# Optimization experiments

Hardware: AMD Instinct MI355X
Metric: run time of the kernel (lower is better)

## Reference

```python
import jax, jax.numpy as jnp
import numpy as np

B, M, E, H, TOPK = 1024, 10000, 8, 512, 2


def setup_inputs() -> dict:
    key = jax.random.key(0)
    ks = jax.random.split(key, 6)
    s_in = 1.0 / np.sqrt(M)
    s_h = 1.0 / np.sqrt(H)
    x = jax.random.normal(ks[0], (B, M), dtype=jnp.float32)
    # Expert params, torch Linear layout stacked over experts
    W1 = jax.random.uniform(ks[1], (E, H, M), jnp.float32, -s_in, s_in)
    b1 = jax.random.uniform(ks[2], (E, H), jnp.float32, -s_in, s_in)
    W2 = jax.random.uniform(ks[3], (E, M, H), jnp.float32, -s_h, s_h)
    b2 = jax.random.uniform(ks[4], (E, M), jnp.float32, -s_h, s_h)
    Wr = jax.random.uniform(ks[5], (E, M), jnp.float32, -s_in, s_in)  # router, no bias
    return {"x": x, "W1": W1, "b1": b1, "W2": W2, "b2": b2, "Wr": Wr}


def reference(x, W1, b1, W2, b2, Wr):
    # Router: logits [B, E], sparse top-k softmax weights scattered to dense [B, E]
    logits = jnp.einsum('bm,em->be', x, Wr)
    topk_vals, topk_idx = jax.lax.top_k(logits, TOPK)
    probs = jax.nn.softmax(topk_vals, axis=-1)
    rw = jnp.zeros_like(logits).at[jnp.arange(B)[:, None], topk_idx].set(probs)
    # Dense all-expert MLP (faithful to original: every expert runs on every token)
    h = jax.nn.relu(jnp.einsum('bm,ehm->beh', x, W1) + b1)      # [B, E, H]
    eo = jnp.einsum('beh,emh->bem', h, W2) + b2                  # [B, E, M]
    # Masked weighted combine
    out = jnp.sum(rw[:, :, None] * eo, axis=1)                   # [B, M]
    return out
```

## Files before the change

kernel.cpp:

```cpp
#include <hip/hip_runtime.h>
#include <hip/hip_bf16.h>


#define B_TOK 1024
#define M_DIM 10000
#define E_NUM 8
#define H_DIM 512
#define NSTEP 313

typedef __attribute__((ext_vector_type(4))) float fx4;
typedef __attribute__((ext_vector_type(8))) short sx8;
typedef __attribute__((ext_vector_type(4))) short sx4;

#define LSTR 40
#define BUFS (256 * LSTR)

__device__ __forceinline__ short f2bf(float f) {
  union { __hip_bfloat16 h; short s; } u;
  u.h = __float2bfloat16(f);
  return u.s;
}

__device__ __forceinline__ sx8 pack8(fx4 a, fx4 b) {
  sx8 r;
  r[0] = f2bf(a[0]); r[1] = f2bf(a[1]); r[2] = f2bf(a[2]); r[3] = f2bf(a[3]);
  r[4] = f2bf(b[0]); r[5] = f2bf(b[1]); r[6] = f2bf(b[2]); r[7] = f2bf(b[3]);
  return r;
}

__global__ void k_zero(int* cnt, int* cnt2) {
  if (threadIdx.x < E_NUM) cnt[threadIdx.x] = 0;
  if (threadIdx.x < 2 * E_NUM) cnt2[threadIdx.x] = 0;
}

__global__ __launch_bounds__(256) void k_router(
    const float* __restrict__ x, const float* __restrict__ Wr,
    int* __restrict__ cnt, int* __restrict__ cnt2,
    int* __restrict__ tokAll, int* __restrict__ qlist2, float* __restrict__ wlist2)
{
  int b = blockIdx.x, t = threadIdx.x;
  const float* xr = x + (size_t)b * M_DIM;
  double acc[E_NUM];
#pragma unroll
  for (int e = 0; e < E_NUM; e++) acc[e] = 0.0;
  for (int m = t; m < M_DIM; m += 256) {
    float xv = xr[m];
#pragma unroll
    for (int e = 0; e < E_NUM; e++)
      acc[e] += (double)xv * (double)Wr[e * M_DIM + m];
  }
#pragma unroll
  for (int e = 0; e < E_NUM; e++) {
#pragma unroll
    for (int off = 32; off > 0; off >>= 1)
      acc[e] += __shfl_xor(acc[e], off);
  }
  __shared__ double part[4][E_NUM];
  int wave = t >> 6;
  if ((t & 63) == 0) {
    for (int e = 0; e < E_NUM; e++) part[wave][e] = acc[e];
  }
  __syncthreads();
  if (t == 0) {
    double lg[E_NUM];
    for (int e = 0; e < E_NUM; e++)
      lg[e] = part[0][e] + part[1][e] + part[2][e] + part[3][e];
    int i0 = 0;
    for (int e = 1; e < E_NUM; e++) if (lg[e] > lg[i0]) i0 = e;
    int i1 = (i0 == 0) ? 1 : 0;
    for (int e = 0; e < E_NUM; e++) if (e != i0 && lg[e] > lg[i1]) i1 = e;
    double ex = exp(lg[i1] - lg[i0]);
    float p0 = (float)(1.0 / (1.0 + ex));
    float p1 = (float)(ex / (1.0 + ex));
    int q0 = atomicAdd(&cnt[i0], 1);
    tokAll[i0 * B_TOK + q0] = b;
    int j0 = atomicAdd(&cnt2[i0 * 2 + 0], 1);
    qlist2[(i0 * 2 + 0) * B_TOK + j0] = q0;
    wlist2[(i0 * 2 + 0) * B_TOK + j0] = p0;
    int q1 = atomicAdd(&cnt[i1], 1);
    tokAll[i1 * B_TOK + q1] = b;
    int j1 = atomicAdd(&cnt2[i1 * 2 + 1], 1);
    qlist2[(i1 * 2 + 1) * B_TOK + j1] = q1;
    wlist2[(i1 * 2 + 1) * B_TOK + j1] = p1;
  }
}

__global__ __launch_bounds__(256) void k_mlp1(
    const float* __restrict__ x, const float* __restrict__ W1,
    const int* __restrict__ cnt, const int* __restrict__ tokAll,
    float* __restrict__ partials, int CH)
{
  int e = blockIdx.z;
  int tt = blockIdx.y >> 2, nt = blockIdx.y & 3;
  int kc = blockIdx.x;

  __shared__ int sh_ne, sh_eoff;
  __shared__ __align__(16) short SB[2 * BUFS];
  __shared__ int toks[128];

  int t = threadIdx.x;
  if (t == 0) {
    int off = 0;
    for (int k = 0; k < e; k++) off += cnt[k];
    sh_eoff = off; sh_ne = cnt[e];
  }
  __syncthreads();
  int ne = sh_ne, eoff = sh_eoff, row0 = tt * 128;
  if (row0 >= ne) return;
  int nvalid = min(128, ne - row0);

  if (t < 128) toks[t] = tokAll[e * B_TOK + row0 + min(t, nvalid - 1)];
  __syncthreads();

  int r4 = t >> 2, kch = t & 3;
  const float* xr0 = x + (size_t)toks[r4] * M_DIM;
  const float* xr1 = x + (size_t)toks[r4 + 64] * M_DIM;
  const float* wr0 = W1 + ((size_t)e * H_DIM + nt * 128 + r4) * M_DIM;
  const float* wr1 = W1 + ((size_t)e * H_DIM + nt * 128 + r4 + 64) * M_DIM;

  int lane = t & 63, wave = t >> 6;
  int wr = wave >> 1, wc = wave & 1;
  int lrow = lane & 15, khalf = lane >> 4;

  fx4 z4 = {0.f, 0.f, 0.f, 0.f};
  fx4 acc[4][4];
#pragma unroll
  for (int m = 0; m < 4; m++)
#pragma unroll
    for (int n = 0; n < 4; n++) acc[m][n] = z4;

  int s0 = kc * CH, s1 = min(s0 + CH, NSTEP);
  sx8 zv = {0, 0, 0, 0, 0, 0, 0, 0};

  {
    int off = s0 * 32 + kch * 8;
    int oc = min(off, M_DIM - 8);
    bool ok = (off + 8 <= M_DIM);
    fx4 A0 = *(const fx4*)(xr0 + oc), A0b = *(const fx4*)(xr0 + oc + 4);
    fx4 A1 = *(const fx4*)(xr1 + oc), A1b = *(const fx4*)(xr1 + oc + 4);
    fx4 B0 = *(const fx4*)(wr0 + oc), B0b = *(const fx4*)(wr0 + oc + 4);
    fx4 B1 = *(const fx4*)(wr1 + oc), B1b = *(const fx4*)(wr1 + oc + 4);
    sx8 pa0 = ok ? pack8(A0, A0b) : zv;
    sx8 pa1 = ok ? pack8(A1, A1b) : zv;
    sx8 pb0 = ok ? pack8(B0, B0b) : zv;
    sx8 pb1 = ok ? pack8(B1, B1b) : zv;
    *(sx8*)(&SB[r4 * LSTR + kch * 8]) = pa0;
    *(sx8*)(&SB[(r4 + 64) * LSTR + kch * 8]) = pa1;
    *(sx8*)(&SB[(128 + r4) * LSTR + kch * 8]) = pb0;
    *(sx8*)(&SB[(128 + r4 + 64) * LSTR + kch * 8]) = pb1;
  }
  __syncthreads();

  int c = 0;
  for (int s = s0; s < s1; s++) {
    int off = (s + 1) * 32 + kch * 8;
    int oc = min(off, M_DIM - 8);
    bool okn = (off + 8 <= M_DIM);
    fx4 A0 = *(const fx4*)(xr0 + oc), A0b = *(const fx4*)(xr0 + oc + 4);
    fx4 A1 = *(const fx4*)(xr1 + oc), A1b = *(const fx4*)(xr1 + oc + 4);
    fx4 B0 = *(const fx4*)(wr0 + oc), B0b = *(const fx4*)(wr0 + oc + 4);
    fx4 B1 = *(const fx4*)(wr1 + oc), B1b = *(const fx4*)(wr1 + oc + 4);

    int bo = c * BUFS;
    sx8 af[4], bf[4];
#pragma unroll
    for (int m = 0; m < 4; m++)
      af[m] = *(const sx8*)(&SB[bo + (wr * 64 + m * 16 + lrow) * LSTR + khalf * 8]);
#pragma unroll
    for (int n = 0; n < 4; n++)
      bf[n] = *(const sx8*)(&SB[bo + (128 + wc * 64 + n * 16 + lrow) * LSTR + khalf * 8]);
#pragma unroll
    for (int m = 0; m < 4; m++)
#pragma unroll
      for (int n = 0; n < 4; n++)
        acc[m][n] = __builtin_amdgcn_mfma_f32_16x16x32_bf16(af[m], bf[n], acc[m][n], 0, 0, 0);

    if (s + 1 < s1) {
      int wo = (c ^ 1) * BUFS;
      sx8 pa0 = okn ? pack8(A0, A0b) : zv;
      sx8 pa1 = okn ? pack8(A1, A1b) : zv;
      sx8 pb0 = okn ? pack8(B0, B0b) : zv;
      sx8 pb1 = okn ? pack8(B1, B1b) : zv;
      *(sx8*)(&SB[wo + r4 * LSTR + kch * 8]) = pa0;
      *(sx8*)(&SB[wo + (r4 + 64) * LSTR + kch * 8]) = pa1;
      *(sx8*)(&SB[wo + (128 + r4) * LSTR + kch * 8]) = pb0;
      *(sx8*)(&SB[wo + (128 + r4 + 64) * LSTR + kch * 8]) = pb1;
    }
    __syncthreads();
    c ^= 1;
  }

#pragma unroll
  for (int m = 0; m < 4; m++)
#pragma unroll
    for (int n = 0; n < 4; n++) {
      int colg = nt * 128 + wc * 64 + n * 16 + lrow;
#pragma unroll
      for (int r = 0; r < 4; r++) {
        int rl = wr * 64 + m * 16 + khalf * 4 + r;
        if (rl < nvalid) {
          int grow = eoff + row0 + rl;
          partials[((size_t)kc * 2048 + grow) * H_DIM + colg] = acc[m][n][r];
        }
      }
    }
}

__global__ __launch_bounds__(256) void k_hreduce(
    const float* __restrict__ partials, const float* __restrict__ b1,
    const int* __restrict__ cnt, short* __restrict__ hbuf, int KC)
{
  __shared__ int sc[E_NUM];
  int t = threadIdx.x;
  if (t < E_NUM) sc[t] = cnt[t];
  __syncthreads();
  int i = (blockIdx.x * 256 + t) * 4;
  int slot = i >> 9;
  int e = 0, off = 0;
  for (int k = 0; k < E_NUM - 1; k++) {
    if (slot >= off + sc[k]) { off += sc[k]; e++; } else break;
  }
  fx4 v = *(const fx4*)(partials + i);
  for (int kc = 1; kc < KC; kc++)
    v += *(const fx4*)(partials + (size_t)kc * 2048 * H_DIM + i);
  fx4 bv = *(const fx4*)(b1 + e * H_DIM + (i & (H_DIM - 1)));
  sx4 o;
#pragma unroll
  for (int j = 0; j < 4; j++) o[j] = f2bf(fmaxf(v[j] + bv[j], 0.f));
  *(sx4*)(hbuf + i) = o;
}

__global__ __launch_bounds__(256) void k_mlp2(
    const short* __restrict__ hbuf, const float* __restrict__ W2,
    const float* __restrict__ b2, const int* __restrict__ cnt,
    const int* __restrict__ cnt2, const int* __restrict__ tokAll,
    const int* __restrict__ qlist2, const float* __restrict__ wlist2,
    float* __restrict__ out, int ord)
{
  int e = blockIdx.z, mt = blockIdx.y, tt = blockIdx.x;

  __shared__ int sh_ne2, sh_eoff;
  __shared__ __align__(16) short SB[2 * BUFS];
  __shared__ int sl[128];
  __shared__ int tok2[128];
  __shared__ float wts[128];

  int t = threadIdx.x;
  if (t == 0) {
    int off = 0;
    for (int k = 0; k < e; k++) off += cnt[k];
    sh_eoff = off; sh_ne2 = cnt2[e * 2 + ord];
  }
  __syncthreads();
  int ne2 = sh_ne2, eoff = sh_eoff, row0 = tt * 128;
  if (row0 >= ne2) return;
  int nvalid = min(128, ne2 - row0);

  if (t < 128) {
    int j = row0 + min(t, nvalid - 1);
    int q = qlist2[(e * 2 + ord) * B_TOK + j];
    sl[t] = eoff + q;
    tok2[t] = tokAll[e * B_TOK + q];
    wts[t] = (t < nvalid) ? wlist2[(e * 2 + ord) * B_TOK + j] : 0.f;
  }
  __syncthreads();

  int r4 = t >> 2, kch = t & 3;
  const short* hr0 = hbuf + (size_t)sl[r4] * H_DIM;
  const short* hr1 = hbuf + (size_t)sl[r4 + 64] * H_DIM;
  const float* w20 = W2 + ((size_t)e * M_DIM + min(mt * 128 + r4, M_DIM - 1)) * H_DIM;
  const float* w21 = W2 + ((size_t)e * M_DIM + min(mt * 128 + r4 + 64, M_DIM - 1)) * H_DIM;

  int lane = t & 63, wave = t >> 6;
  int wr = wave >> 1, wc = wave & 1;
  int lrow = lane & 15, khalf = lane >> 4;

  fx4 z4 = {0.f, 0.f, 0.f, 0.f};
  fx4 acc[4][4];
#pragma unroll
  for (int m = 0; m < 4; m++)
#pragma unroll
    for (int n = 0; n < 4; n++) acc[m][n] = z4;

  {
    int off = kch * 8;
    sx8 pa0 = *(const sx8*)(hr0 + off);
    sx8 pa1 = *(const sx8*)(hr1 + off);
    fx4 B0 = *(const fx4*)(w20 + off), B0b = *(const fx4*)(w20 + off + 4);
    fx4 B1 = *(const fx4*)(w21 + off), B1b = *(const fx4*)(w21 + off + 4);
    *(sx8*)(&SB[r4 * LSTR + kch * 8]) = pa0;
    *(sx8*)(&SB[(r4 + 64) * LSTR + kch * 8]) = pa1;
    *(sx8*)(&SB[(128 + r4) * LSTR + kch * 8]) = pack8(B0, B0b);
    *(sx8*)(&SB[(128 + r4 + 64) * LSTR + kch * 8]) = pack8(B1, B1b);
  }
  __syncthreads();

  int c = 0;
  for (int s = 0; s < 16; s++) {
    int off = min((s + 1) * 32 + kch * 8, H_DIM - 8);
    sx8 pa0 = *(const sx8*)(hr0 + off);
    sx8 pa1 = *(const sx8*)(hr1 + off);
    fx4 B0 = *(const fx4*)(w20 + off), B0b = *(const fx4*)(w20 + off + 4);
    fx4 B1 = *(const fx4*)(w21 + off), B1b = *(const fx4*)(w21 + off + 4);

    int bo = c * BUFS;
    sx8 af[4], bf[4];
#pragma unroll
    for (int m = 0; m < 4; m++)
      af[m] = *(const sx8*)(&SB[bo + (wr * 64 + m * 16 + lrow) * LSTR + khalf * 8]);
#pragma unroll
    for (int n = 0; n < 4; n++)
      bf[n] = *(const sx8*)(&SB[bo + (128 + wc * 64 + n * 16 + lrow) * LSTR + khalf * 8]);
#pragma unroll
    for (int m = 0; m < 4; m++)
#pragma unroll
      for (int n = 0; n < 4; n++)
        acc[m][n] = __builtin_amdgcn_mfma_f32_16x16x32_bf16(af[m], bf[n], acc[m][n], 0, 0, 0);

    if (s + 1 < 16) {
      int wo = (c ^ 1) * BUFS;
      *(sx8*)(&SB[wo + r4 * LSTR + kch * 8]) = pa0;
      *(sx8*)(&SB[wo + (r4 + 64) * LSTR + kch * 8]) = pa1;
      *(sx8*)(&SB[wo + (128 + r4) * LSTR + kch * 8]) = pack8(B0, B0b);
      *(sx8*)(&SB[wo + (128 + r4 + 64) * LSTR + kch * 8]) = pack8(B1, B1b);
    }
    __syncthreads();
    c ^= 1;
  }

#pragma unroll
  for (int m = 0; m < 4; m++)
#pragma unroll
    for (int n = 0; n < 4; n++) {
      int colg = mt * 128 + wc * 64 + n * 16 + lrow;
      if (colg < M_DIM) {
        float b2v = b2[(size_t)e * M_DIM + colg];
#pragma unroll
        for (int r = 0; r < 4; r++) {
          int rl = wr * 64 + m * 16 + khalf * 4 + r;
          if (rl < nvalid) {
            float v = wts[rl] * (acc[m][n][r] + b2v);
            float* dst = out + (size_t)tok2[rl] * M_DIM + colg;
            if (ord == 0) *dst = v;
            else *dst += v;
          }
        }
      }
    }
}

extern "C" void kernel_launch(void* const* d_in, const int* in_sizes, int n_in,
                              void* d_out, int out_size, void* d_ws, size_t ws_size,
                              hipStream_t stream) {
  const float* x  = (const float*)d_in[0];
  const float* W1 = (const float*)d_in[1];
  const float* b1 = (const float*)d_in[2];
  const float* W2 = (const float*)d_in[3];
  const float* b2 = (const float*)d_in[4];
  const float* Wr = (const float*)d_in[5];
  float* out = (float*)d_out;

  int KC = (ws_size >= (size_t)36 * 1024 * 1024) ? 8 : 4;
  int CH = (NSTEP + KC - 1) / KC;

  char* p = (char*)d_ws;
  float* partials = (float*)p;               p += (size_t)KC * 2048 * H_DIM * 4;
  short* hbuf     = (short*)p;               p += (size_t)2048 * H_DIM * 2;
  int*   cnt      = (int*)p;                 p += 64;
  int*   cnt2     = (int*)p;                 p += 64;
  int*   tokAll   = (int*)p;                 p += E_NUM * B_TOK * 4;
  int*   qlist2   = (int*)p;                 p += 2 * E_NUM * B_TOK * 4;
  float* wlist2   = (float*)p;

  k_zero<<<1, 64, 0, stream>>>(cnt, cnt2);
  k_router<<<B_TOK, 256, 0, stream>>>(x, Wr, cnt, cnt2, tokAll, qlist2, wlist2);
  k_mlp1<<<dim3(KC, 12, E_NUM), 256, 0, stream>>>(x, W1, cnt, tokAll, partials, CH);
  k_hreduce<<<1024, 256, 0, stream>>>(partials, b1, cnt, hbuf, KC);
  k_mlp2<<<dim3(2, 79, E_NUM), 256, 0, stream>>>(hbuf, W2, b2, cnt, cnt2, tokAll,
                                                 qlist2, wlist2, out, 0);
  k_mlp2<<<dim3(2, 79, E_NUM), 256, 0, stream>>>(hbuf, W2, b2, cnt, cnt2, tokAll,
                                                 qlist2, wlist2, out, 1);
}
```

Baseline: 359.5 us.

## Pre-convert weights and activations to bf16 and load tiles via global_load_lds

When the workspace is large enough, x is converted to bf16 inside the router, and W1 and W2 are each converted to bf16 by a separate pass every call. New GEMM kernels then stream the bf16 tiles straight into LDS with global_load_lds double buffering, instead of converting fp32 to bf16 inside the MLP loops. This is meant to cut conversion work and register staging in the GEMM inner loops. In exchange it adds full fp32 read and bf16 write passes over roughly 330 MB of weights on every call, plus a large workspace requirement.

```diff
diff --git a/kernel.cpp b/kernel.cpp
--- a/kernel.cpp
+++ b/kernel.cpp
@@ -28,26 +28,54 @@
   return r;
 }
 
-__global__ void k_zero(int* cnt, int* cnt2) {
+__device__ __forceinline__ void gload16(const short* g, short* l) {
+  __builtin_amdgcn_global_load_lds(
+      (const __attribute__((address_space(1))) void*)g,
+      (__attribute__((address_space(3))) void*)l, 16, 0, 0);
+}
+
+__global__ void k_zero(int* cnt, int* cnt2, int* zpad) {
   if (threadIdx.x < E_NUM) cnt[threadIdx.x] = 0;
   if (threadIdx.x < 2 * E_NUM) cnt2[threadIdx.x] = 0;
+  if (threadIdx.x < 16) zpad[threadIdx.x] = 0;
+}
+
+__global__ __launch_bounds__(256) void k_cvt(
+    const float* __restrict__ src, short* __restrict__ dst)
+{
+  size_t i = ((size_t)blockIdx.x * 256 + threadIdx.x) * 8;
+  fx4 a = *(const fx4*)(src + i);
+  fx4 b = *(const fx4*)(src + i + 4);
+  *(sx8*)(dst + i) = pack8(a, b);
 }
 
 __global__ __launch_bounds__(256) void k_router(
     const float* __restrict__ x, const float* __restrict__ Wr,
     int* __restrict__ cnt, int* __restrict__ cnt2,
-    int* __restrict__ tokAll, int* __restrict__ qlist2, float* __restrict__ wlist2)
+    int* __restrict__ tokAll, int* __restrict__ qlist2, float* __restrict__ wlist2,
+    short* __restrict__ xb)
 {
   int b = blockIdx.x, t = threadIdx.x;
   const float* xr = x + (size_t)b * M_DIM;
   double acc[E_NUM];
 #pragma unroll
   for (int e = 0; e < E_NUM; e++) acc[e] = 0.0;
-  for (int m = t; m < M_DIM; m += 256) {
-    float xv = xr[m];
-#pragma unroll
-    for (int e = 0; e < E_NUM; e++)
-      acc[e] += (double)xv * (double)Wr[e * M_DIM + m];
+  if (xb) {
+    short* xbr = xb + (size_t)b * M_DIM;
+    for (int m = t; m < M_DIM; m += 256) {
+      float xv = xr[m];
+      xbr[m] = f2bf(xv);
+#pragma unroll
+      for (int e = 0; e < E_NUM; e++)
+        acc[e] += (double)xv * (double)Wr[e * M_DIM + m];
+    }
+  } else {
+    for (int m = t; m < M_DIM; m += 256) {
+      float xv = xr[m];
+#pragma unroll
+      for (int e = 0; e < E_NUM; e++)
+        acc[e] += (double)xv * (double)Wr[e * M_DIM + m];
+    }
   }
 #pragma unroll
   for (int e = 0; e < E_NUM; e++) {
@@ -85,6 +113,245 @@
   }
 }
 
+
+__global__ __launch_bounds__(256) void k_mlp1g(
+    const short* __restrict__ xb, const short* __restrict__ Wb,
+    const int* __restrict__ cnt, const int* __restrict__ tokAll,
+    float* __restrict__ partials, const short* __restrict__ zpad, int CH)
+{
+  int e = blockIdx.z;
+  int tt = blockIdx.y >> 2, nt = blockIdx.y & 3;
+  int kc = blockIdx.x;
+
+  __shared__ int sh_ne, sh_eoff;
+  __shared__ __align__(16) short LA[2][4096];
+  __shared__ __align__(16) short LB[2][4096];
+  __shared__ int toks[128];
+
+  int t = threadIdx.x;
+  if (t == 0) {
+    int off = 0;
+    for (int k = 0; k < e; k++) off += cnt[k];
+    sh_eoff = off; sh_ne = cnt[e];
+  }
+  __syncthreads();
+  int ne = sh_ne, eoff = sh_eoff, row0 = tt * 128;
+  if (row0 >= ne) return;
+  int nvalid = min(128, ne - row0);
+  if (t < 128) toks[t] = tokAll[e * B_TOK + row0 + min(t, nvalid - 1)];
+  __syncthreads();
+
+  int lane = t & 63, wave = t >> 6;
+  int srow = wave * 32 + (lane >> 2);
+  int scol = (lane & 3) * 8;
+  const short* ap0 = xb + (size_t)toks[srow] * M_DIM + scol;
+  const short* ap1 = xb + (size_t)toks[srow + 16] * M_DIM + scol;
+  const short* bp0 = Wb + ((size_t)e * H_DIM + nt * 128 + srow) * M_DIM + scol;
+  const short* bp1 = bp0 + (size_t)16 * M_DIM;
+  int ld0 = (wave * 32) * 32;
+  int ld1 = (wave * 32 + 16) * 32;
+
+  int wr = wave >> 1, wc = wave & 1;
+  int lrow = lane & 15, khalf = lane >> 4;
+
+  fx4 z4 = {0.f, 0.f, 0.f, 0.f};
+  fx4 acc[4][4];
+#pragma unroll
+  for (int m = 0; m < 4; m++)
+#pragma unroll
+    for (int n = 0; n < 4; n++) acc[m][n] = z4;
+
+  int s0 = kc * CH, s1 = min(s0 + CH, NSTEP);
+
+  {
+    int ko = s0 * 32;
+    bool ok = (ko + scol + 8 <= M_DIM);
+    gload16(ok ? (ap0 + ko) : zpad, LA[0] + ld0);
+    gload16(ok ? (ap1 + ko) : zpad, LA[0] + ld1);
+    gload16(ok ? (bp0 + ko) : zpad, LB[0] + ld0);
+    gload16(ok ? (bp1 + ko) : zpad, LB[0] + ld1);
+  }
+  __syncthreads();
+
+  int c = 0;
+  for (int s = s0; s < s1; s++) {
+    if (s + 1 < s1) {
+      int ko = (s + 1) * 32;
+      bool ok = (ko + scol + 8 <= M_DIM);
+      int cn = c ^ 1;
+      gload16(ok ? (ap0 + ko) : zpad, LA[cn] + ld0);
+      gload16(ok ? (ap1 + ko) : zpad, LA[cn] + ld1);
+      gload16(ok ? (bp0 + ko) : zpad, LB[cn] + ld0);
+      gload16(ok ? (bp1 + ko) : zpad, LB[cn] + ld1);
+    }
+    sx8 af[4], bf[4];
+#pragma unroll
+    for (int m = 0; m < 4; m++)
+      af[m] = *(const sx8*)(LA[c] + (wr * 64 + m * 16 + lrow) * 32 + khalf * 8);
+#pragma unroll
+    for (int n = 0; n < 4; n++)
+      bf[n] = *(const sx8*)(LB[c] + (wc * 64 + n * 16 + lrow) * 32 + khalf * 8);
+#pragma unroll
+    for (int m = 0; m < 4; m++)
+#pragma unroll
+      for (int n = 0; n < 4; n++)
+        acc[m][n] = __builtin_amdgcn_mfma_f32_16x16x32_bf16(af[m], bf[n], acc[m][n], 0, 0, 0);
+    __syncthreads();
+    c ^= 1;
+  }
+
+#pragma unroll
+  for (int m = 0; m < 4; m++)
+#pragma unroll
+    for (int n = 0; n < 4; n++) {
+      int colg = nt * 128 + wc * 64 + n * 16 + lrow;
+#pragma unroll
+      for (int r = 0; r < 4; r++) {
+        int rl = wr * 64 + m * 16 + khalf * 4 + r;
+        if (rl < nvalid) {
+          int grow = eoff + row0 + rl;
+          partials[((size_t)kc * 2048 + grow) * H_DIM + colg] = acc[m][n][r];
+        }
+      }
+    }
+}
+
+__global__ __launch_bounds__(256) void k_mlp2g(
+    const short* __restrict__ hbuf, const short* __restrict__ Wb,
+    const float* __restrict__ b2, const int* __restrict__ cnt,
+    const int* __restrict__ cnt2, const int* __restrict__ tokAll,
+    const int* __restrict__ qlist2, const float* __restrict__ wlist2,
+    float* __restrict__ out, int ord)
+{
+  int e = blockIdx.z, mt = blockIdx.y, tt = blockIdx.x;
+
+  __shared__ int sh_ne2, sh_eoff;
+  __shared__ __align__(16) short LA[2][4096];
+  __shared__ __align__(16) short LB[2][4096];
+  __shared__ int sl[128];
+  __shared__ int tok2[128];
+  __shared__ float wts[128];
+
+  int t = threadIdx.x;
+  if (t == 0) {
+    int off = 0;
+    for (int k = 0; k < e; k++) off += cnt[k];
+    sh_eoff = off; sh_ne2 = cnt2[e * 2 + ord];
+  }
+  __syncthreads();
+  int ne2 = sh_ne2, eoff = sh_eoff, row0 = tt * 128;
+  if (row0 >= ne2) return;
+  int nvalid = min(128, ne2 - row0);
+
+  if (t < 128) {
+    int j = row0 + min(t, nvalid - 1);
+    int q = qlist2[(e * 2 + ord) * B_TOK + j];
+    sl[t] = eoff + q;
+    tok2[t] = tokAll[e * B_TOK + q];
+    wts[t] = (t < nvalid) ? wlist2[(e * 2 + ord) * B_TOK + j] : 0.f;
+  }
+  __syncthreads();
+
+  int lane = t & 63, wave = t >> 6;
+  int srow = wave * 32 + (lane >> 2);
+  int scol = (lane & 3) * 8;
+  const short* ap0 = hbuf + (size_t)sl[srow] * H_DIM + scol;
+  const short* ap1 = hbuf + (size_t)sl[srow + 16] * H_DIM + scol;
+  const short* bp0 = Wb + ((size_t)e * M_DIM + min(mt * 128 + srow, M_DIM - 1)) * H_DIM + scol;
+  const short* bp1 = Wb + ((size_t)e * M_DIM + min(mt * 128 + srow + 16, M_DIM - 1)) * H_DIM + scol;
+  int ld0 = (wave * 32) * 32;
+  int ld1 = (wave * 32 + 16) * 32;
+
+  int wr = wave >> 1, wc = wave & 1;
+  int lrow = lane & 15, khalf = lane >> 4;
+
+  fx4 z4 = {0.f, 0.f, 0.f, 0.f};
+  fx4 acc[4][4];
+#pragma unroll
+  for (int m = 0; m < 4; m++)
+#pragma unroll
+    for (int n = 0; n < 4; n++) acc[m][n] = z4;
+
+  {
+    gload16(ap0, LA[0] + ld0);
+    gload16(ap1, LA[0] + ld1);
+    gload16(bp0, LB[0] + ld0);
+    gload16(bp1, LB[0] + ld1);
+  }
+  __syncthreads();
+
+  int c = 0;
+  for (int s = 0; s < 16; s++) {
+    if (s + 1 < 16) {
+      int ko = (s + 1) * 32;
+      int cn = c ^ 1;
+      gload16(ap0 + ko, LA[cn] + ld0);
+      gload16(ap1 + ko, LA[cn] + ld1);
+      gload16(bp0 + ko, LB[cn] + ld0);
+      gload16(bp1 + ko, LB[cn] + ld1);
+    }
+    sx8 af[4], bf[4];
+#pragma unroll
+    for (int m = 0; m < 4; m++)
+      af[m] = *(const sx8*)(LA[c] + (wr * 64 + m * 16 + lrow) * 32 + khalf * 8);
+#pragma unroll
+    for (int n = 0; n < 4; n++)
+      bf[n] = *(const sx8*)(LB[c] + (wc * 64 + n * 16 + lrow) * 32 + khalf * 8);
+#pragma unroll
+    for (int m = 0; m < 4; m++)
+#pragma unroll
+      for (int n = 0; n < 4; n++)
+        acc[m][n] = __builtin_amdgcn_mfma_f32_16x16x32_bf16(af[m], bf[n], acc[m][n], 0, 0, 0);
+    __syncthreads();
+    c ^= 1;
+  }
+
+#pragma unroll
+  for (int m = 0; m < 4; m++)
+#pragma unroll
+    for (int n = 0; n < 4; n++) {
+      int colg = mt * 128 + wc * 64 + n * 16 + lrow;
+      if (colg < M_DIM) {
+        float b2v = b2[(size_t)e * M_DIM + colg];
+#pragma unroll
+        for (int r = 0; r < 4; r++) {
+          int rl = wr * 64 + m * 16 + khalf * 4 + r;
+          if (rl < nvalid) {
+            float v = wts[rl] * (acc[m][n][r] + b2v);
+            float* dst = out + (size_t)tok2[rl] * M_DIM + colg;
+            if (ord == 0) *dst = v;
+            else *dst += v;
+          }
+        }
+      }
+    }
+}
+
+__global__ __launch_bounds__(256) void k_hreduce(
+    const float* __restrict__ partials, const float* __restrict__ b1,
+    const int* __restrict__ cnt, short* __restrict__ hbuf, int KC)
+{
+  __shared__ int sc[E_NUM];
+  int t = threadIdx.x;
+  if (t < E_NUM) sc[t] = cnt[t];
+  __syncthreads();
+  int i = (blockIdx.x * 256 + t) * 4;
+  int slot = i >> 9;
+  int e = 0, off = 0;
+  for (int k = 0; k < E_NUM - 1; k++) {
+    if (slot >= off + sc[k]) { off += sc[k]; e++; } else break;
+  }
+  fx4 v = *(const fx4*)(partials + i);
+  for (int kc = 1; kc < KC; kc++)
+    v += *(const fx4*)(partials + (size_t)kc * 2048 * H_DIM + i);
+  fx4 bv = *(const fx4*)(b1 + e * H_DIM + (i & (H_DIM - 1)));
+  sx4 o;
+#pragma unroll
+  for (int j = 0; j < 4; j++) o[j] = f2bf(fmaxf(v[j] + bv[j], 0.f));
+  *(sx4*)(hbuf + i) = o;
+}
+
+
 __global__ __launch_bounds__(256) void k_mlp1(
     const float* __restrict__ x, const float* __restrict__ W1,
     const int* __restrict__ cnt, const int* __restrict__ tokAll,
@@ -136,14 +403,10 @@
     int off = s0 * 32 + kch * 8;
     int oc = min(off, M_DIM - 8);
     bool ok = (off + 8 <= M_DIM);
-    fx4 A0 = *(const fx4*)(xr0 + oc), A0b = *(const fx4*)(xr0 + oc + 4);
-    fx4 A1 = *(const fx4*)(xr1 + oc), A1b = *(const fx4*)(xr1 + oc + 4);
-    fx4 B0 = *(const fx4*)(wr0 + oc), B0b = *(const fx4*)(wr0 + oc + 4);
-    fx4 B1 = *(const fx4*)(wr1 + oc), B1b = *(const fx4*)(wr1 + oc + 4);
-    sx8 pa0 = ok ? pack8(A0, A0b) : zv;
-    sx8 pa1 = ok ? pack8(A1, A1b) : zv;
-    sx8 pb0 = ok ? pack8(B0, B0b) : zv;
-    sx8 pb1 = ok ? pack8(B1, B1b) : zv;
+    sx8 pa0 = ok ? pack8(*(const fx4*)(xr0 + oc), *(const fx4*)(xr0 + oc + 4)) : zv;
+    sx8 pa1 = ok ? pack8(*(const fx4*)(xr1 + oc), *(const fx4*)(xr1 + oc + 4)) : zv;
+    sx8 pb0 = ok ? pack8(*(const fx4*)(wr0 + oc), *(const fx4*)(wr0 + oc + 4)) : zv;
+    sx8 pb1 = ok ? pack8(*(const fx4*)(wr1 + oc), *(const fx4*)(wr1 + oc + 4)) : zv;
     *(sx8*)(&SB[r4 * LSTR + kch * 8]) = pa0;
     *(sx8*)(&SB[(r4 + 64) * LSTR + kch * 8]) = pa1;
     *(sx8*)(&SB[(128 + r4) * LSTR + kch * 8]) = pb0;
@@ -206,30 +469,6 @@
     }
 }
 
-__global__ __launch_bounds__(256) void k_hreduce(
-    const float* __restrict__ partials, const float* __restrict__ b1,
-    const int* __restrict__ cnt, short* __restrict__ hbuf, int KC)
-{
-  __shared__ int sc[E_NUM];
-  int t = threadIdx.x;
-  if (t < E_NUM) sc[t] = cnt[t];
-  __syncthreads();
-  int i = (blockIdx.x * 256 + t) * 4;
-  int slot = i >> 9;
-  int e = 0, off = 0;
-  for (int k = 0; k < E_NUM - 1; k++) {
-    if (slot >= off + sc[k]) { off += sc[k]; e++; } else break;
-  }
-  fx4 v = *(const fx4*)(partials + i);
-  for (int kc = 1; kc < KC; kc++)
-    v += *(const fx4*)(partials + (size_t)kc * 2048 * H_DIM + i);
-  fx4 bv = *(const fx4*)(b1 + e * H_DIM + (i & (H_DIM - 1)));
-  sx4 o;
-#pragma unroll
-  for (int j = 0; j < 4; j++) o[j] = f2bf(fmaxf(v[j] + bv[j], 0.f));
-  *(sx4*)(hbuf + i) = o;
-}
-
 __global__ __launch_bounds__(256) void k_mlp2(
     const short* __restrict__ hbuf, const float* __restrict__ W2,
     const float* __restrict__ b2, const int* __restrict__ cnt,
@@ -360,24 +599,54 @@
   const float* Wr = (const float*)d_in[5];
   float* out = (float*)d_out;
 
-  int KC = (ws_size >= (size_t)36 * 1024 * 1024) ? 8 : 4;
-  int CH = (NSTEP + KC - 1) / KC;
-
-  char* p = (char*)d_ws;
-  float* partials = (float*)p;               p += (size_t)KC * 2048 * H_DIM * 4;
-  short* hbuf     = (short*)p;               p += (size_t)2048 * H_DIM * 2;
-  int*   cnt      = (int*)p;                 p += 64;
-  int*   cnt2     = (int*)p;                 p += 64;
-  int*   tokAll   = (int*)p;                 p += E_NUM * B_TOK * 4;
-  int*   qlist2   = (int*)p;                 p += 2 * E_NUM * B_TOK * 4;
-  float* wlist2   = (float*)p;
-
-  k_zero<<<1, 64, 0, stream>>>(cnt, cnt2);
-  k_router<<<B_TOK, 256, 0, stream>>>(x, Wr, cnt, cnt2, tokAll, qlist2, wlist2);
-  k_mlp1<<<dim3(KC, 12, E_NUM), 256, 0, stream>>>(x, W1, cnt, tokAll, partials, CH);
-  k_hreduce<<<1024, 256, 0, stream>>>(partials, b1, cnt, hbuf, KC);
-  k_mlp2<<<dim3(2, 79, E_NUM), 256, 0, stream>>>(hbuf, W2, b2, cnt, cnt2, tokAll,
-                                                 qlist2, wlist2, out, 0);
-  k_mlp2<<<dim3(2, 79, E_NUM), 256, 0, stream>>>(hbuf, W2, b2, cnt, cnt2, tokAll,
-                                                 qlist2, wlist2, out, 1);
-}
+  const size_t NEED_BF16 = 138215616ULL;
+  int mode = (ws_size >= NEED_BF16) ? 1 : 0;
+
+  if (mode == 1) {
+    const int KC = 8, CH = (NSTEP + KC - 1) / KC;
+    char* p = (char*)d_ws;
+    float* partials = (float*)p;        p += (size_t)KC * 2048 * H_DIM * 4;
+    short* hbuf     = (short*)p;        p += (size_t)2048 * H_DIM * 2;
+    int*   cnt      = (int*)p;          p += 64;
+    int*   cnt2     = (int*)p;          p += 64;
+    int*   tokAll   = (int*)p;          p += E_NUM * B_TOK * 4;
+    int*   qlist2   = (int*)p;          p += 2 * E_NUM * B_TOK * 4;
+    float* wlist2   = (float*)p;        p += 2 * E_NUM * B_TOK * 4;
+    int*   zpad     = (int*)p;          p += 64;
+    short* xb       = (short*)p;        p += (size_t)B_TOK * M_DIM * 2;
+    short* Wb       = (short*)p;
+
+    k_zero<<<1, 64, 0, stream>>>(cnt, cnt2, zpad);
+    k_router<<<B_TOK, 256, 0, stream>>>(x, Wr, cnt, cnt2, tokAll, qlist2, wlist2, xb);
+    k_cvt<<<20000, 256, 0, stream>>>(W1, Wb);
+    k_mlp1g<<<dim3(KC, 12, E_NUM), 256, 0, stream>>>(xb, Wb, cnt, tokAll, partials,
+                                                     (const short*)zpad, CH);
+    k_hreduce<<<1024, 256, 0, stream>>>(partials, b1, cnt, hbuf, KC);
+    k_cvt<<<20000, 256, 0, stream>>>(W2, Wb);
+    k_mlp2g<<<dim3(2, 79, E_NUM), 256, 0, stream>>>(hbuf, Wb, b2, cnt, cnt2, tokAll,
+                                                    qlist2, wlist2, out, 0);
+    k_mlp2g<<<dim3(2, 79, E_NUM), 256, 0, stream>>>(hbuf, Wb, b2, cnt, cnt2, tokAll,
+                                                    qlist2, wlist2, out, 1);
+  } else {
+    int KC = (ws_size >= (size_t)36 * 1024 * 1024) ? 8 : 4;
+    int CH = (NSTEP + KC - 1) / KC;
+    char* p = (char*)d_ws;
+    float* partials = (float*)p;        p += (size_t)KC * 2048 * H_DIM * 4;
+    short* hbuf     = (short*)p;        p += (size_t)2048 * H_DIM * 2;
+    int*   cnt      = (int*)p;          p += 64;
+    int*   cnt2     = (int*)p;          p += 64;
+    int*   tokAll   = (int*)p;          p += E_NUM * B_TOK * 4;
+    int*   qlist2   = (int*)p;          p += 2 * E_NUM * B_TOK * 4;
+    float* wlist2   = (float*)p;        p += 2 * E_NUM * B_TOK * 4;
+    int*   zpad     = (int*)p;
+
+    k_zero<<<1, 64, 0, stream>>>(cnt, cnt2, zpad);
+    k_router<<<B_TOK, 256, 0, stream>>>(x, Wr, cnt, cnt2, tokAll, qlist2, wlist2, nullptr);
+    k_mlp1<<<dim3(KC, 12, E_NUM), 256, 0, stream>>>(x, W1, cnt, tokAll, partials, CH);
+    k_hreduce<<<1024, 256, 0, stream>>>(partials, b1, cnt, hbuf, KC);
+    k_mlp2<<<dim3(2, 79, E_NUM), 256, 0, stream>>>(hbuf, W2, b2, cnt, cnt2, tokAll,
+                                                   qlist2, wlist2, out, 0);
+    k_mlp2<<<dim3(2, 79, E_NUM), 256, 0, stream>>>(hbuf, W2, b2, cnt, cnt2, tokAll,
+                                                   qlist2, wlist2, out, 1);
+  }
+}
```

After: 388.1 us. 1.08x slower.
